# Performance work log

Hardware: AMD Instinct MI355X
Metric: run time of the kernel (lower is better)

## Reference

```python
import jax, jax.numpy as jnp
import numpy as np
import math

B, S, D, H = 2, 2048, 1024, 16
DK = D // H

def setup_inputs() -> dict:
    key = jax.random.key(0)
    ks = jax.random.split(key, 12)
    def xavier(k, shape):
        fan_in, fan_out = shape[1], shape[0]
        limit = math.sqrt(6.0 / (fan_in + fan_out))
        return jax.random.uniform(k, shape, jnp.float32, -limit, limit)
    inp = {
        'query': jax.random.normal(ks[0], (B, S, D), jnp.float32),
        'key':   jax.random.normal(ks[1], (B, S, D), jnp.float32),
        'value': jax.random.normal(ks[2], (B, S, D), jnp.float32),
        # causal mask, broadcast over heads: (B, 1, S, S), 1 = keep, 0 = mask
        'mask':  jnp.broadcast_to(jnp.tril(jnp.ones((S, S), jnp.int32)), (B, 1, S, S)),
        'Wq': xavier(ks[3], (D, D)), 'bq': jnp.zeros((D,), jnp.float32),
        'Wk': xavier(ks[4], (D, D)), 'bk': jnp.zeros((D,), jnp.float32),
        'Wv': xavier(ks[5], (D, D)), 'bv': jnp.zeros((D,), jnp.float32),
        'Wo': xavier(ks[6], (D, D)), 'bo': jnp.zeros((D,), jnp.float32),
    }
    return inp

def _split_heads(x):
    # (B, S, D) -> (B, H, S, DK)
    b, s, _ = x.shape
    return x.reshape(b, s, H, DK).transpose(0, 2, 1, 3)

def reference(query, key, value, mask, Wq, bq, Wk, bk, Wv, bv, Wo, bo):
    # torch nn.Linear: y = x @ W.T + b
    Q = _split_heads(query @ Wq.T + bq)   # (B,H,S,DK)
    K = _split_heads(key   @ Wk.T + bk)
    V = _split_heads(value @ Wv.T + bv)
    scores = jnp.einsum('bhqd,bhkd->bhqk', Q, K) / math.sqrt(DK)  # (B,H,S,S)
    scores = jnp.where(mask == 0, jnp.float32(-1e9), scores)
    attn = jax.nn.softmax(scores, axis=-1)  # dropout p=0 -> identity
    out = jnp.einsum('bhqk,bhkd->bhqd', attn, V)  # (B,H,S,DK)
    out = out.transpose(0, 2, 1, 3).reshape(query.shape[0], query.shape[1], D)
    return out @ Wo.T + bo
```

## Files before the change

kernel.cpp:

```cpp
#include <hip/hip_runtime.h>
#include <hip/hip_bf16.h>
#include <type_traits>


typedef __attribute__((ext_vector_type(8))) short short8;
typedef __attribute__((ext_vector_type(4))) short s16x4;
typedef __attribute__((ext_vector_type(4))) float floatx4;

__device__ __forceinline__ short f2bf(float x) {
    union { float f; unsigned u; } v; v.f = x;
    unsigned r = v.u + 0x7fffu + ((v.u >> 16) & 1u);
    return (short)(r >> 16);
}

__device__ __forceinline__ unsigned pk2bf(float a, float b) {
    union { __hip_bfloat162 h2; unsigned u; } cv;
    cv.h2 = __float22bfloat162_rn(make_float2(a, b));
    return cv.u;
}

__device__ __forceinline__ float fast_exp2(float x) {
#if __has_builtin(__builtin_amdgcn_exp2f)
    return __builtin_amdgcn_exp2f(x);
#else
    return __expf(x * 0.69314718056f);
#endif
}

typedef __attribute__((address_space(3))) short lds_short;
typedef __attribute__((address_space(1))) const short glb_short;
__device__ __forceinline__ void load_lds16(const void* g, void* l) {
    __builtin_amdgcn_global_load_lds((glb_short*)g, (lds_short*)l, 16, 0, 0);
}

__global__ __launch_bounds__(256) void cvt_all(
        const float* __restrict__ q, const float* __restrict__ k,
        const float* __restrict__ v,
        const float* __restrict__ wq, const float* __restrict__ wk,
        const float* __restrict__ wv, const float* __restrict__ wo,
        unsigned short* __restrict__ xq, unsigned short* __restrict__ xk,
        unsigned short* __restrict__ xv,
        unsigned short* __restrict__ wqb, unsigned short* __restrict__ wkb,
        unsigned short* __restrict__ wvb, unsigned short* __restrict__ wob) {
    const float* s; unsigned short* d;
    int bx = blockIdx.x;
    switch (blockIdx.y) {
        case 0: s = q; d = xq; break;
        case 1: s = k; d = xk; break;
        case 2: s = v; d = xv; break;
        default: {
            int wsel = bx >> 9; bx &= 511;
            s = (wsel == 0) ? wq : (wsel == 1) ? wk : (wsel == 2) ? wv : wo;
            d = (wsel == 0) ? wqb : (wsel == 1) ? wkb : (wsel == 2) ? wvb : wob;
        }
    }
    size_t i = ((size_t)bx * 256 + threadIdx.x) * 8;
    floatx4 a = *(const floatx4*)(s + i), b2 = *(const floatx4*)(s + i + 4);
    union { unsigned u[4]; short8 v8; } o;
    o.u[0] = pk2bf(a[0], a[1]);  o.u[1] = pk2bf(a[2], a[3]);
    o.u[2] = pk2bf(b2[0], b2[1]); o.u[3] = pk2bf(b2[2], b2[3]);
    *(short8*)(d + i) = o.v8;
}

__global__ __launch_bounds__(256) void gemm_qkv(
        const unsigned short* __restrict__ Xq, const unsigned short* __restrict__ Xk,
        const unsigned short* __restrict__ Xv,
        const unsigned short* __restrict__ Wq, const unsigned short* __restrict__ Wk,
        const unsigned short* __restrict__ Wv,
        const float* __restrict__ bq, const float* __restrict__ bk,
        const float* __restrict__ bv,
        unsigned short* __restrict__ Qb, unsigned short* __restrict__ Kb,
        unsigned short* __restrict__ Vb) {
    constexpr int K = 1024, N = 1024;
    __shared__ short As[128 * 64];
    __shared__ short Bs[128 * 64];
    const int t = threadIdx.x;
    const int chunk = blockIdx.y >> 5, my = blockIdx.y & 31;
    const unsigned short* A = chunk == 0 ? Xq : chunk == 1 ? Xk : Xv;
    const unsigned short* W = chunk == 0 ? Wq : chunk == 1 ? Wk : Wv;
    const float* bias        = chunk == 0 ? bq : chunk == 1 ? bk : bv;
    unsigned short* Y        = chunk == 0 ? Qb : chunk == 1 ? Kb : Vb;
    const float scale = chunk == 0 ? 0.1803368801f : 1.0f;
    const int m0 = my * 128, n0 = blockIdx.x * 128;
    const int lane = t & 63, w = t >> 6;
    const int l16 = lane & 15, quad = lane >> 4;
    const int wm = w >> 1, wn = w & 1;
    const int srow8 = t >> 3, scs8 = t & 7;
    floatx4 acc[4][4] = {};

    for (int k0 = 0; k0 < K; k0 += 64) {
        __syncthreads();
        for (int i = 0; i < 4; i++) {
            const int row = i * 32 + srow8;
            const int cg = scs8 ^ (row & 7);
            load_lds16(A + (size_t)(m0 + row) * K + k0 + cg * 8, &As[i * 2048 + t * 8]);
            load_lds16(W + (size_t)(n0 + row) * K + k0 + cg * 8, &Bs[i * 2048 + t * 8]);
        }
        __syncthreads();

        for (int kc = 0; kc < 2; kc++) {
            short8 af[4], bf[4];
            for (int ms = 0; ms < 4; ms++) {
                const int row = wm * 64 + ms * 16 + l16;
                af[ms] = *(short8*)&As[row * 64 + (((kc << 2) | quad) ^ (row & 7)) * 8];
            }
            for (int ns = 0; ns < 4; ns++) {
                const int row = wn * 64 + ns * 16 + l16;
                bf[ns] = *(short8*)&Bs[row * 64 + (((kc << 2) | quad) ^ (row & 7)) * 8];
            }
            for (int ms = 0; ms < 4; ms++)
                for (int ns = 0; ns < 4; ns++)
                    acc[ms][ns] = __builtin_amdgcn_mfma_f32_16x16x32_bf16(
                            af[ms], bf[ns], acc[ms][ns], 0, 0, 0);
        }
    }

    for (int ms = 0; ms < 4; ms++)
        for (int ns = 0; ns < 4; ns++) {
            int col = n0 + wn * 64 + ns * 16 + l16;
            float bb = bias[col];
            for (int r = 0; r < 4; r++) {
                int row = m0 + wm * 64 + ms * 16 + quad * 4 + r;
                Y[(size_t)row * N + col] =
                    (unsigned short)f2bf((acc[ms][ns][r] + bb) * scale);
            }
        }
}

__global__ __launch_bounds__(256) void gemm_o(
        const unsigned short* __restrict__ A, const unsigned short* __restrict__ W,
        float* __restrict__ P) {
    constexpr int K = 1024, N = 1024;
    __shared__ short As[128 * 64];
    __shared__ short Bs[128 * 64];
    const int t = threadIdx.x;
    const int m0 = blockIdx.y * 128, n0 = blockIdx.x * 128;
    const int kz = blockIdx.z;
    const int lane = t & 63, w = t >> 6;
    const int l16 = lane & 15, quad = lane >> 4;
    const int wm = w >> 1, wn = w & 1;
    const int srow8 = t >> 3, scs8 = t & 7;
    floatx4 acc[4][4] = {};

    for (int k0 = kz * 512; k0 < kz * 512 + 512; k0 += 64) {
        __syncthreads();
        for (int i = 0; i < 4; i++) {
            const int row = i * 32 + srow8;
            const int cg = scs8 ^ (row & 7);
            load_lds16(A + (size_t)(m0 + row) * K + k0 + cg * 8, &As[i * 2048 + t * 8]);
            load_lds16(W + (size_t)(n0 + row) * K + k0 + cg * 8, &Bs[i * 2048 + t * 8]);
        }
        __syncthreads();

        for (int kc = 0; kc < 2; kc++) {
            short8 af[4], bf[4];
            for (int ms = 0; ms < 4; ms++) {
                const int row = wm * 64 + ms * 16 + l16;
                af[ms] = *(short8*)&As[row * 64 + (((kc << 2) | quad) ^ (row & 7)) * 8];
            }
            for (int ns = 0; ns < 4; ns++) {
                const int row = wn * 64 + ns * 16 + l16;
                bf[ns] = *(short8*)&Bs[row * 64 + (((kc << 2) | quad) ^ (row & 7)) * 8];
            }
            for (int ms = 0; ms < 4; ms++)
                for (int ns = 0; ns < 4; ns++)
                    acc[ms][ns] = __builtin_amdgcn_mfma_f32_16x16x32_bf16(
                            af[ms], bf[ns], acc[ms][ns], 0, 0, 0);
        }
    }

    float* Pz = P + (size_t)kz * 4096 * N;
    for (int ms = 0; ms < 4; ms++)
        for (int ns = 0; ns < 4; ns++) {
            int col = n0 + wn * 64 + ns * 16 + l16;
            for (int r = 0; r < 4; r++) {
                int row = m0 + wm * 64 + ms * 16 + quad * 4 + r;
                Pz[(size_t)row * N + col] = acc[ms][ns][r];
            }
        }
}

__global__ __launch_bounds__(256) void reduce_o(const float* __restrict__ P,
        const float* __restrict__ bo, float* __restrict__ out) {
    size_t i = ((size_t)blockIdx.x * 256 + threadIdx.x) * 4;
    floatx4 a = *(const floatx4*)(P + i);
    floatx4 b = *(const floatx4*)(P + (size_t)4096 * 1024 + i);
    floatx4 bb = *(const floatx4*)(bo + (i & 1023));
    *(floatx4*)(out + i) = a + b + bb;
}

__global__ __launch_bounds__(256) void attn_kernel(
        const unsigned short* __restrict__ Q, const unsigned short* __restrict__ Kp,
        const unsigned short* __restrict__ Vp, unsigned short* __restrict__ O) {
    __shared__ short Ks[64 * 72];
    __shared__ short Vt[64 * 72];
    __shared__ short PsA[4][16 * 70];
    __shared__ short PsB[4][16 * 70];
    const int t = threadIdx.x;
    const int bx = blockIdx.x;
    const int unit = bx & 15, h = (bx >> 4) & 15, b = bx >> 8;
    const int q0A = unit * 64, q0B = (31 - unit) * 64;
    const int lane = t & 63, w = t >> 6, l16 = lane & 15, quad = lane >> 4;
    const int krow = t >> 2, kcg = (t & 3) * 16;
    const int vp2 = t & 31, vg = t >> 5;

    short8 qfA[2], qfB[2];
    {
        const size_t baseA = ((size_t)(b * 2048 + q0A + w * 16 + l16)) * 1024 + h * 64;
        qfA[0] = *(const short8*)(Q + baseA + quad * 8);
        qfA[1] = *(const short8*)(Q + baseA + 32 + quad * 8);
        const size_t baseB = ((size_t)(b * 2048 + q0B + w * 16 + l16)) * 1024 + h * 64;
        qfB[0] = *(const short8*)(Q + baseB + quad * 8);
        qfB[1] = *(const short8*)(Q + baseB + 32 + quad * 8);
    }
    float lA = 0.f, lB = 0.f;
    floatx4 oA[4] = {}, oB[4] = {};

    short8 ka, kb, va, vc;
    {
        const size_t kbse = ((size_t)(b * 2048 + krow)) * 1024 + h * 64 + kcg;
        ka = *(const short8*)(Kp + kbse);
        kb = *(const short8*)(Kp + kbse + 8);
        const size_t vbse = ((size_t)(b * 2048 + 2 * vp2)) * 1024 + h * 64 + vg * 8;
        va = *(const short8*)(Vp + vbse);
        vc = *(const short8*)(Vp + vbse + 1024);
    }

    for (int kv0 = 0; kv0 < q0B + 64; kv0 += 64) {
        __syncthreads();
        *(short8*)&Ks[krow * 72 + kcg] = ka;
        *(short8*)&Ks[krow * 72 + kcg + 8] = kb;
        for (int i = 0; i < 8; i++) {
            unsigned pk = (unsigned)(unsigned short)va[i] |
                          ((unsigned)(unsigned short)vc[i] << 16);
            *(unsigned*)&Vt[(vg * 8 + i) * 72 + 2 * vp2] = pk;
        }
        __syncthreads();

        if (kv0 < q0B) {
            const size_t kbse = ((size_t)(b * 2048 + kv0 + 64 + krow)) * 1024 + h * 64 + kcg;
            ka = *(const short8*)(Kp + kbse);
            kb = *(const short8*)(Kp + kbse + 8);
            const size_t vbse = ((size_t)(b * 2048 + kv0 + 64 + 2 * vp2)) * 1024 + h * 64 + vg * 8;
            va = *(const short8*)(Vp + vbse);
            vc = *(const short8*)(Vp + vbse + 1024);
        }

        auto body = [&](auto dual_c) {
            constexpr bool DUAL = decltype(dual_c)::value;
            floatx4 sB[4] = {};
            floatx4 sA[4];
            if constexpr (DUAL)
                for (int i = 0; i < 4; i++) sA[i] = (floatx4){0.f, 0.f, 0.f, 0.f};
            for (int hh = 0; hh < 4; hh++)
                for (int kc = 0; kc < 2; kc++) {
                    short8 kf = *(short8*)&Ks[(hh * 16 + l16) * 72 + kc * 32 + quad * 8];
                    sB[hh] = __builtin_amdgcn_mfma_f32_16x16x32_bf16(kf, qfB[kc], sB[hh], 0, 0, 0);
                    if constexpr (DUAL)
                        sA[hh] = __builtin_amdgcn_mfma_f32_16x16x32_bf16(kf, qfA[kc], sA[hh], 0, 0, 0);
                }

            {
                const bool needmask = (kv0 + 63 > q0B + w * 16);
                const int qg = q0B + w * 16 + l16;
                float ls = 0.f;
                for (int hh = 0; hh < 4; hh++) {
                    float p[4];
                    for (int r = 0; r < 4; r++) {
                        int kv = kv0 + hh * 16 + quad * 4 + r;
                        float e = fast_exp2(sB[hh][r]);
                        p[r] = (needmask && kv > qg) ? 0.f : e;
                        ls += p[r];
                    }
                    union { unsigned u[2]; s16x4 v4; } pw;
                    pw.u[0] = pk2bf(p[0], p[1]); pw.u[1] = pk2bf(p[2], p[3]);
                    *(s16x4*)&PsB[w][l16 * 70 + hh * 16 + quad * 4] = pw.v4;
                }
                ls += __shfl_xor(ls, 16);
                ls += __shfl_xor(ls, 32);
                lB += ls;
            }
            if constexpr (DUAL) {
                const bool needmask = (kv0 + 63 > q0A + w * 16);
                const int qg = q0A + w * 16 + l16;
                float ls = 0.f;
                for (int hh = 0; hh < 4; hh++) {
                    float p[4];
                    for (int r = 0; r < 4; r++) {
                        int kv = kv0 + hh * 16 + quad * 4 + r;
                        float e = fast_exp2(sA[hh][r]);
                        p[r] = (needmask && kv > qg) ? 0.f : e;
                        ls += p[r];
                    }
                    union { unsigned u[2]; s16x4 v4; } pw;
                    pw.u[0] = pk2bf(p[0], p[1]); pw.u[1] = pk2bf(p[2], p[3]);
                    *(s16x4*)&PsA[w][l16 * 70 + hh * 16 + quad * 4] = pw.v4;
                }
                ls += __shfl_xor(ls, 16);
                ls += __shfl_xor(ls, 32);
                lA += ls;
            }

            short8 pB0 = *(short8*)&PsB[w][l16 * 70 + quad * 8];
            short8 pB1 = *(short8*)&PsB[w][l16 * 70 + 32 + quad * 8];
            short8 pA0, pA1;
            if constexpr (DUAL) {
                pA0 = *(short8*)&PsA[w][l16 * 70 + quad * 8];
                pA1 = *(short8*)&PsA[w][l16 * 70 + 32 + quad * 8];
            }
            for (int nc = 0; nc < 4; nc++) {
                short8 vf0 = *(short8*)&Vt[(nc * 16 + l16) * 72 + quad * 8];
                short8 vf1 = *(short8*)&Vt[(nc * 16 + l16) * 72 + 32 + quad * 8];
                oB[nc] = __builtin_amdgcn_mfma_f32_16x16x32_bf16(vf0, pB0, oB[nc], 0, 0, 0);
                oB[nc] = __builtin_amdgcn_mfma_f32_16x16x32_bf16(vf1, pB1, oB[nc], 0, 0, 0);
                if constexpr (DUAL) {
                    oA[nc] = __builtin_amdgcn_mfma_f32_16x16x32_bf16(vf0, pA0, oA[nc], 0, 0, 0);
                    oA[nc] = __builtin_amdgcn_mfma_f32_16x16x32_bf16(vf1, pA1, oA[nc], 0, 0, 0);
                }
            }
        };
        if (kv0 <= q0A) body(std::integral_constant<bool, true>{});
        else            body(std::integral_constant<bool, false>{});
    }

    {
        const float rl = 1.f / lB;
        const size_t orow = ((size_t)(b * 2048 + q0B + w * 16 + l16)) * 1024 + h * 64;
        for (int nc = 0; nc < 4; nc++) {
            union { unsigned u[2]; s16x4 v4; } ow;
            ow.u[0] = pk2bf(oB[nc][0] * rl, oB[nc][1] * rl);
            ow.u[1] = pk2bf(oB[nc][2] * rl, oB[nc][3] * rl);
            *(s16x4*)(O + orow + nc * 16 + quad * 4) = ow.v4;
        }
    }
    {
        const float rl = 1.f / lA;
        const size_t orow = ((size_t)(b * 2048 + q0A + w * 16 + l16)) * 1024 + h * 64;
        for (int nc = 0; nc < 4; nc++) {
            union { unsigned u[2]; s16x4 v4; } ow;
            ow.u[0] = pk2bf(oA[nc][0] * rl, oA[nc][1] * rl);
            ow.u[1] = pk2bf(oA[nc][2] * rl, oA[nc][3] * rl);
            *(s16x4*)(O + orow + nc * 16 + quad * 4) = ow.v4;
        }
    }
}

extern "C" void kernel_launch(void* const* d_in, const int* in_sizes, int n_in,
                              void* d_out, int out_size, void* d_ws, size_t ws_size,
                              hipStream_t stream) {
    const float* query = (const float*)d_in[0];
    const float* key   = (const float*)d_in[1];
    const float* value = (const float*)d_in[2];
    const float* Wq = (const float*)d_in[4];
    const float* bq = (const float*)d_in[5];
    const float* Wk = (const float*)d_in[6];
    const float* bk = (const float*)d_in[7];
    const float* Wv = (const float*)d_in[8];
    const float* bv = (const float*)d_in[9];
    const float* Wo = (const float*)d_in[10];
    const float* bo = (const float*)d_in[11];

    const size_t NE = (size_t)4096 * 1024;
    const size_t WE = (size_t)1024 * 1024;
    unsigned short* Xq  = (unsigned short*)d_ws;
    unsigned short* Xk  = Xq + NE;
    unsigned short* Xv  = Xk + NE;
    unsigned short* Qb  = Xv + NE;
    unsigned short* Kb  = Qb + NE;
    unsigned short* Vb  = Kb + NE;
    unsigned short* Ob  = Vb + NE;
    unsigned short* Wqb = Ob + NE;
    unsigned short* Wkb = Wqb + WE;
    unsigned short* Wvb = Wkb + WE;
    unsigned short* Wob = Wvb + WE;
    float* Opart = (float*)d_ws;

    cvt_all<<<dim3(2048, 4), 256, 0, stream>>>(query, key, value, Wq, Wk, Wv, Wo,
                                               Xq, Xk, Xv, Wqb, Wkb, Wvb, Wob);
    gemm_qkv<<<dim3(8, 96), 256, 0, stream>>>(Xq, Xk, Xv, Wqb, Wkb, Wvb,
                                              bq, bk, bv, Qb, Kb, Vb);
    attn_kernel<<<dim3(512), 256, 0, stream>>>(Qb, Kb, Vb, Ob);
    gemm_o<<<dim3(8, 32, 2), 256, 0, stream>>>(Ob, Wob, Opart);
    reduce_o<<<dim3(4096), 256, 0, stream>>>(Opart, bo, (float*)d_out);
}
```

Baseline: 257.8 us.

## Split attention KV range across two blocks and drop split-K in output GEMM

The attention kernel now splits each query pair's key/value tiles between two blocks (even and odd tiles), doubling the grid to 1024 blocks. Each block writes unnormalized fp32 partial outputs and row sums, and a new combine kernel adds the halves, normalizes and converts to bf16. The output projection GEMM switches from split-K with a separate reduce kernel to 64x64 tiles over the full K, with the bias folded into its epilogue. The aim is more parallelism in attention at the cost of an extra fp32 round trip through memory. Splitting without a running max is only valid because neither half rescales against a max, so both partial sums share the same scale.

```diff
diff --git a/kernel.cpp b/kernel.cpp
--- a/kernel.cpp
+++ b/kernel.cpp
@@ -129,22 +129,21 @@
 
 __global__ __launch_bounds__(256) void gemm_o(
         const unsigned short* __restrict__ A, const unsigned short* __restrict__ W,
-        float* __restrict__ P) {
+        const float* __restrict__ bias, float* __restrict__ out) {
     constexpr int K = 1024, N = 1024;
-    __shared__ short As[128 * 64];
-    __shared__ short Bs[128 * 64];
+    __shared__ short As[64 * 64];
+    __shared__ short Bs[64 * 64];
     const int t = threadIdx.x;
-    const int m0 = blockIdx.y * 128, n0 = blockIdx.x * 128;
-    const int kz = blockIdx.z;
+    const int m0 = blockIdx.y * 64, n0 = blockIdx.x * 64;
     const int lane = t & 63, w = t >> 6;
     const int l16 = lane & 15, quad = lane >> 4;
     const int wm = w >> 1, wn = w & 1;
     const int srow8 = t >> 3, scs8 = t & 7;
-    floatx4 acc[4][4] = {};
-
-    for (int k0 = kz * 512; k0 < kz * 512 + 512; k0 += 64) {
-        __syncthreads();
-        for (int i = 0; i < 4; i++) {
+    floatx4 acc[2][2] = {};
+
+    for (int k0 = 0; k0 < K; k0 += 64) {
+        __syncthreads();
+        for (int i = 0; i < 2; i++) {
             const int row = i * 32 + srow8;
             const int cg = scs8 ^ (row & 7);
             load_lds16(A + (size_t)(m0 + row) * K + k0 + cg * 8, &As[i * 2048 + t * 8]);
@@ -153,53 +152,46 @@
         __syncthreads();
 
         for (int kc = 0; kc < 2; kc++) {
-            short8 af[4], bf[4];
-            for (int ms = 0; ms < 4; ms++) {
-                const int row = wm * 64 + ms * 16 + l16;
+            short8 af[2], bf[2];
+            for (int ms = 0; ms < 2; ms++) {
+                const int row = wm * 32 + ms * 16 + l16;
                 af[ms] = *(short8*)&As[row * 64 + (((kc << 2) | quad) ^ (row & 7)) * 8];
             }
-            for (int ns = 0; ns < 4; ns++) {
-                const int row = wn * 64 + ns * 16 + l16;
+            for (int ns = 0; ns < 2; ns++) {
+                const int row = wn * 32 + ns * 16 + l16;
                 bf[ns] = *(short8*)&Bs[row * 64 + (((kc << 2) | quad) ^ (row & 7)) * 8];
             }
-            for (int ms = 0; ms < 4; ms++)
-                for (int ns = 0; ns < 4; ns++)
+            for (int ms = 0; ms < 2; ms++)
+                for (int ns = 0; ns < 2; ns++)
                     acc[ms][ns] = __builtin_amdgcn_mfma_f32_16x16x32_bf16(
                             af[ms], bf[ns], acc[ms][ns], 0, 0, 0);
         }
     }
 
-    float* Pz = P + (size_t)kz * 4096 * N;
-    for (int ms = 0; ms < 4; ms++)
-        for (int ns = 0; ns < 4; ns++) {
-            int col = n0 + wn * 64 + ns * 16 + l16;
+    for (int ms = 0; ms < 2; ms++)
+        for (int ns = 0; ns < 2; ns++) {
+            int col = n0 + wn * 32 + ns * 16 + l16;
+            float bb = bias[col];
             for (int r = 0; r < 4; r++) {
-                int row = m0 + wm * 64 + ms * 16 + quad * 4 + r;
-                Pz[(size_t)row * N + col] = acc[ms][ns][r];
-            }
-        }
-}
-
-__global__ __launch_bounds__(256) void reduce_o(const float* __restrict__ P,
-        const float* __restrict__ bo, float* __restrict__ out) {
-    size_t i = ((size_t)blockIdx.x * 256 + threadIdx.x) * 4;
-    floatx4 a = *(const floatx4*)(P + i);
-    floatx4 b = *(const floatx4*)(P + (size_t)4096 * 1024 + i);
-    floatx4 bb = *(const floatx4*)(bo + (i & 1023));
-    *(floatx4*)(out + i) = a + b + bb;
+                int row = m0 + wm * 32 + ms * 16 + quad * 4 + r;
+                out[(size_t)row * N + col] = acc[ms][ns][r] + bb;
+            }
+        }
 }
 
 __global__ __launch_bounds__(256) void attn_kernel(
         const unsigned short* __restrict__ Q, const unsigned short* __restrict__ Kp,
-        const unsigned short* __restrict__ Vp, unsigned short* __restrict__ O) {
+        const unsigned short* __restrict__ Vp, float* __restrict__ Opart,
+        float* __restrict__ Lpart) {
     __shared__ short Ks[64 * 72];
     __shared__ short Vt[64 * 72];
     __shared__ short PsA[4][16 * 70];
     __shared__ short PsB[4][16 * 70];
     const int t = threadIdx.x;
     const int bx = blockIdx.x;
-    const int unit = bx & 15, h = (bx >> 4) & 15, b = bx >> 8;
+    const int unit = bx & 15, h = (bx >> 4) & 15, half = (bx >> 8) & 1, b = bx >> 9;
     const int q0A = unit * 64, q0B = (31 - unit) * 64;
+    const int nB = 32 - unit;
     const int lane = t & 63, w = t >> 6, l16 = lane & 15, quad = lane >> 4;
     const int krow = t >> 2, kcg = (t & 3) * 16;
     const int vp2 = t & 31, vg = t >> 5;
@@ -218,15 +210,16 @@
 
     short8 ka, kb, va, vc;
     {
-        const size_t kbse = ((size_t)(b * 2048 + krow)) * 1024 + h * 64 + kcg;
+        const size_t kbse = ((size_t)(b * 2048 + half * 64 + krow)) * 1024 + h * 64 + kcg;
         ka = *(const short8*)(Kp + kbse);
         kb = *(const short8*)(Kp + kbse + 8);
-        const size_t vbse = ((size_t)(b * 2048 + 2 * vp2)) * 1024 + h * 64 + vg * 8;
+        const size_t vbse = ((size_t)(b * 2048 + half * 64 + 2 * vp2)) * 1024 + h * 64 + vg * 8;
         va = *(const short8*)(Vp + vbse);
         vc = *(const short8*)(Vp + vbse + 1024);
     }
 
-    for (int kv0 = 0; kv0 < q0B + 64; kv0 += 64) {
+    for (int kvt = half; kvt < nB; kvt += 2) {
+        const int kv0 = kvt * 64;
         __syncthreads();
         *(short8*)&Ks[krow * 72 + kcg] = ka;
         *(short8*)&Ks[krow * 72 + kcg + 8] = kb;
@@ -237,11 +230,12 @@
         }
         __syncthreads();
 
-        if (kv0 < q0B) {
-            const size_t kbse = ((size_t)(b * 2048 + kv0 + 64 + krow)) * 1024 + h * 64 + kcg;
+        if (kvt + 2 < nB) {
+            const int nx = (kvt + 2) * 64;
+            const size_t kbse = ((size_t)(b * 2048 + nx + krow)) * 1024 + h * 64 + kcg;
             ka = *(const short8*)(Kp + kbse);
             kb = *(const short8*)(Kp + kbse + 8);
-            const size_t vbse = ((size_t)(b * 2048 + kv0 + 64 + 2 * vp2)) * 1024 + h * 64 + vg * 8;
+            const size_t vbse = ((size_t)(b * 2048 + nx + 2 * vp2)) * 1024 + h * 64 + vg * 8;
             va = *(const short8*)(Vp + vbse);
             vc = *(const short8*)(Vp + vbse + 1024);
         }
@@ -323,26 +317,34 @@
         else            body(std::integral_constant<bool, false>{});
     }
 
+    float* Oh = Opart + (size_t)half * 4194304;
     {
-        const float rl = 1.f / lB;
-        const size_t orow = ((size_t)(b * 2048 + q0B + w * 16 + l16)) * 1024 + h * 64;
-        for (int nc = 0; nc < 4; nc++) {
-            union { unsigned u[2]; s16x4 v4; } ow;
-            ow.u[0] = pk2bf(oB[nc][0] * rl, oB[nc][1] * rl);
-            ow.u[1] = pk2bf(oB[nc][2] * rl, oB[nc][3] * rl);
-            *(s16x4*)(O + orow + nc * 16 + quad * 4) = ow.v4;
-        }
+        const int rowg = b * 2048 + q0B + w * 16 + l16;
+        float* Op = Oh + (size_t)rowg * 1024 + h * 64;
+        for (int nc = 0; nc < 4; nc++)
+            *(floatx4*)(Op + nc * 16 + quad * 4) = oB[nc];
+        if (quad == 0) Lpart[half * 65536 + rowg * 16 + h] = lB;
     }
     {
-        const float rl = 1.f / lA;
-        const size_t orow = ((size_t)(b * 2048 + q0A + w * 16 + l16)) * 1024 + h * 64;
-        for (int nc = 0; nc < 4; nc++) {
-            union { unsigned u[2]; s16x4 v4; } ow;
-            ow.u[0] = pk2bf(oA[nc][0] * rl, oA[nc][1] * rl);
-            ow.u[1] = pk2bf(oA[nc][2] * rl, oA[nc][3] * rl);
-            *(s16x4*)(O + orow + nc * 16 + quad * 4) = ow.v4;
-        }
-    }
+        const int rowg = b * 2048 + q0A + w * 16 + l16;
+        float* Op = Oh + (size_t)rowg * 1024 + h * 64;
+        for (int nc = 0; nc < 4; nc++)
+            *(floatx4*)(Op + nc * 16 + quad * 4) = oA[nc];
+        if (quad == 0) Lpart[half * 65536 + rowg * 16 + h] = lA;
+    }
+}
+
+__global__ __launch_bounds__(256) void combine_o(const float* __restrict__ Op,
+        const float* __restrict__ Lp, unsigned short* __restrict__ Ob) {
+    size_t i = ((size_t)blockIdx.x * 256 + threadIdx.x) * 4;
+    int row = (int)(i >> 10), h = ((int)i >> 6) & 15;
+    floatx4 a = *(const floatx4*)(Op + i);
+    floatx4 b = *(const floatx4*)(Op + 4194304 + i);
+    float rl = 1.f / (Lp[row * 16 + h] + Lp[65536 + row * 16 + h]);
+    union { unsigned u[2]; s16x4 v4; } ow;
+    ow.u[0] = pk2bf((a[0] + b[0]) * rl, (a[1] + b[1]) * rl);
+    ow.u[1] = pk2bf((a[2] + b[2]) * rl, (a[3] + b[3]) * rl);
+    *(s16x4*)(Ob + i) = ow.v4;
 }
 
 extern "C" void kernel_launch(void* const* d_in, const int* in_sizes, int n_in,
@@ -360,26 +362,26 @@
     const float* Wo = (const float*)d_in[10];
     const float* bo = (const float*)d_in[11];
 
-    const size_t NE = (size_t)4096 * 1024;
-    const size_t WE = (size_t)1024 * 1024;
-    unsigned short* Xq  = (unsigned short*)d_ws;
-    unsigned short* Xk  = Xq + NE;
-    unsigned short* Xv  = Xk + NE;
-    unsigned short* Qb  = Xv + NE;
-    unsigned short* Kb  = Qb + NE;
-    unsigned short* Vb  = Kb + NE;
-    unsigned short* Ob  = Vb + NE;
-    unsigned short* Wqb = Ob + NE;
-    unsigned short* Wkb = Wqb + WE;
-    unsigned short* Wvb = Wkb + WE;
-    unsigned short* Wob = Wvb + WE;
-    float* Opart = (float*)d_ws;
+    unsigned short* base = (unsigned short*)d_ws;
+    unsigned short* Qb  = base;
+    unsigned short* Kb  = base + 4194304;
+    unsigned short* Vb  = base + 8388608;
+    unsigned short* Ob  = Kb;
+    unsigned short* Wob = base + 12582912;
+    float* Lpart = (float*)(base + 13631488);
+    float* Opart = (float*)((char*)d_ws + (size_t)28 * 1024 * 1024);
+    unsigned short* Xq  = base + 14680064;
+    unsigned short* Xk  = base + 18874368;
+    unsigned short* Xv  = base + 23068672;
+    unsigned short* Wqb = base + 27262976;
+    unsigned short* Wkb = base + 28311552;
+    unsigned short* Wvb = base + 29360128;
 
     cvt_all<<<dim3(2048, 4), 256, 0, stream>>>(query, key, value, Wq, Wk, Wv, Wo,
                                                Xq, Xk, Xv, Wqb, Wkb, Wvb, Wob);
     gemm_qkv<<<dim3(8, 96), 256, 0, stream>>>(Xq, Xk, Xv, Wqb, Wkb, Wvb,
                                               bq, bk, bv, Qb, Kb, Vb);
-    attn_kernel<<<dim3(512), 256, 0, stream>>>(Qb, Kb, Vb, Ob);
-    gemm_o<<<dim3(8, 32, 2), 256, 0, stream>>>(Ob, Wob, Opart);
-    reduce_o<<<dim3(4096), 256, 0, stream>>>(Opart, bo, (float*)d_out);
-}
+    attn_kernel<<<dim3(1024), 256, 0, stream>>>(Qb, Kb, Vb, Opart, Lpart);
+    combine_o<<<dim3(4096), 256, 0, stream>>>(Opart, Lpart, Ob);
+    gemm_o<<<dim3(16, 64), 256, 0, stream>>>(Ob, Wob, bo, (float*)d_out);
+}
```

After: 259.7 us. No clear change (+0.8%).

## Fuse activation bf16 conversion into QKV GEMM and drop split-K output reduction

Applied to the files above, without the earlier changes.

The QKV projection GEMM now reads fp32 activations directly, converting them to bf16 in registers with a one-tile register prefetch before storing to LDS. This removes the separate conversion pass over the three activation tensors. The output projection switches from a 128x128 split-K GEMM plus a reduce kernel to 64x64 tiles over the full K, with the bias added in the epilogue. That removes the fp32 partial-sum round trip and one launch, at the cost of synchronous global loads in the QKV loop and smaller, less reuse-efficient tiles in the output GEMM.

```diff
diff --git a/kernel.cpp b/kernel.cpp
--- a/kernel.cpp
+++ b/kernel.cpp
@@ -33,38 +33,29 @@
     __builtin_amdgcn_global_load_lds((glb_short*)g, (lds_short*)l, 16, 0, 0);
 }
 
-__global__ __launch_bounds__(256) void cvt_all(
-        const float* __restrict__ q, const float* __restrict__ k,
-        const float* __restrict__ v,
-        const float* __restrict__ wq, const float* __restrict__ wk,
-        const float* __restrict__ wv, const float* __restrict__ wo,
-        unsigned short* __restrict__ xq, unsigned short* __restrict__ xk,
-        unsigned short* __restrict__ xv,
-        unsigned short* __restrict__ wqb, unsigned short* __restrict__ wkb,
-        unsigned short* __restrict__ wvb, unsigned short* __restrict__ wob) {
+__global__ __launch_bounds__(256) void cvt_w(
+        const float* __restrict__ s0, const float* __restrict__ s1,
+        const float* __restrict__ s2, const float* __restrict__ s3,
+        unsigned short* __restrict__ d0, unsigned short* __restrict__ d1,
+        unsigned short* __restrict__ d2, unsigned short* __restrict__ d3) {
     const float* s; unsigned short* d;
-    int bx = blockIdx.x;
     switch (blockIdx.y) {
-        case 0: s = q; d = xq; break;
-        case 1: s = k; d = xk; break;
-        case 2: s = v; d = xv; break;
-        default: {
-            int wsel = bx >> 9; bx &= 511;
-            s = (wsel == 0) ? wq : (wsel == 1) ? wk : (wsel == 2) ? wv : wo;
-            d = (wsel == 0) ? wqb : (wsel == 1) ? wkb : (wsel == 2) ? wvb : wob;
-        }
-    }
-    size_t i = ((size_t)bx * 256 + threadIdx.x) * 8;
+        case 0: s = s0; d = d0; break;
+        case 1: s = s1; d = d1; break;
+        case 2: s = s2; d = d2; break;
+        default: s = s3; d = d3; break;
+    }
+    size_t i = ((size_t)blockIdx.x * 256 + threadIdx.x) * 8;
     floatx4 a = *(const floatx4*)(s + i), b2 = *(const floatx4*)(s + i + 4);
     union { unsigned u[4]; short8 v8; } o;
-    o.u[0] = pk2bf(a[0], a[1]);  o.u[1] = pk2bf(a[2], a[3]);
+    o.u[0] = pk2bf(a[0], a[1]);   o.u[1] = pk2bf(a[2], a[3]);
     o.u[2] = pk2bf(b2[0], b2[1]); o.u[3] = pk2bf(b2[2], b2[3]);
     *(short8*)(d + i) = o.v8;
 }
 
 __global__ __launch_bounds__(256) void gemm_qkv(
-        const unsigned short* __restrict__ Xq, const unsigned short* __restrict__ Xk,
-        const unsigned short* __restrict__ Xv,
+        const float* __restrict__ Xq, const float* __restrict__ Xk,
+        const float* __restrict__ Xv,
         const unsigned short* __restrict__ Wq, const unsigned short* __restrict__ Wk,
         const unsigned short* __restrict__ Wv,
         const float* __restrict__ bq, const float* __restrict__ bk,
@@ -76,10 +67,10 @@
     __shared__ short Bs[128 * 64];
     const int t = threadIdx.x;
     const int chunk = blockIdx.y >> 5, my = blockIdx.y & 31;
-    const unsigned short* A = chunk == 0 ? Xq : chunk == 1 ? Xk : Xv;
+    const float* A    = chunk == 0 ? Xq : chunk == 1 ? Xk : Xv;
     const unsigned short* W = chunk == 0 ? Wq : chunk == 1 ? Wk : Wv;
-    const float* bias        = chunk == 0 ? bq : chunk == 1 ? bk : bv;
-    unsigned short* Y        = chunk == 0 ? Qb : chunk == 1 ? Kb : Vb;
+    const float* bias = chunk == 0 ? bq : chunk == 1 ? bk : bv;
+    unsigned short* Y = chunk == 0 ? Qb : chunk == 1 ? Kb : Vb;
     const float scale = chunk == 0 ? 0.1803368801f : 1.0f;
     const int m0 = my * 128, n0 = blockIdx.x * 128;
     const int lane = t & 63, w = t >> 6;
@@ -88,13 +79,37 @@
     const int srow8 = t >> 3, scs8 = t & 7;
     floatx4 acc[4][4] = {};
 
+    floatx4 pa[4][2];
+    for (int i = 0; i < 4; i++) {
+        const int row = i * 32 + srow8;
+        const float* ap = A + (size_t)(m0 + row) * K + (scs8 ^ (row & 7)) * 8;
+        pa[i][0] = *(const floatx4*)ap;
+        pa[i][1] = *(const floatx4*)(ap + 4);
+    }
+
     for (int k0 = 0; k0 < K; k0 += 64) {
         __syncthreads();
         for (int i = 0; i < 4; i++) {
             const int row = i * 32 + srow8;
-            const int cg = scs8 ^ (row & 7);
-            load_lds16(A + (size_t)(m0 + row) * K + k0 + cg * 8, &As[i * 2048 + t * 8]);
-            load_lds16(W + (size_t)(n0 + row) * K + k0 + cg * 8, &Bs[i * 2048 + t * 8]);
+            load_lds16(W + (size_t)(n0 + row) * K + k0 + ((scs8 ^ (row & 7))) * 8,
+                       &Bs[i * 2048 + t * 8]);
+        }
+        for (int i = 0; i < 4; i++) {
+            union { unsigned u[4]; short8 v8; } o;
+            o.u[0] = pk2bf(pa[i][0][0], pa[i][0][1]);
+            o.u[1] = pk2bf(pa[i][0][2], pa[i][0][3]);
+            o.u[2] = pk2bf(pa[i][1][0], pa[i][1][1]);
+            o.u[3] = pk2bf(pa[i][1][2], pa[i][1][3]);
+            *(short8*)&As[i * 2048 + t * 8] = o.v8;
+        }
+        if (k0 + 64 < K) {
+            for (int i = 0; i < 4; i++) {
+                const int row = i * 32 + srow8;
+                const float* ap = A + (size_t)(m0 + row) * K + (k0 + 64) +
+                                  (scs8 ^ (row & 7)) * 8;
+                pa[i][0] = *(const floatx4*)ap;
+                pa[i][1] = *(const floatx4*)(ap + 4);
+            }
         }
         __syncthreads();
 
@@ -129,22 +144,21 @@
 
 __global__ __launch_bounds__(256) void gemm_o(
         const unsigned short* __restrict__ A, const unsigned short* __restrict__ W,
-        float* __restrict__ P) {
+        const float* __restrict__ bias, float* __restrict__ out) {
     constexpr int K = 1024, N = 1024;
-    __shared__ short As[128 * 64];
-    __shared__ short Bs[128 * 64];
+    __shared__ short As[64 * 64];
+    __shared__ short Bs[64 * 64];
     const int t = threadIdx.x;
-    const int m0 = blockIdx.y * 128, n0 = blockIdx.x * 128;
-    const int kz = blockIdx.z;
+    const int m0 = blockIdx.y * 64, n0 = blockIdx.x * 64;
     const int lane = t & 63, w = t >> 6;
     const int l16 = lane & 15, quad = lane >> 4;
     const int wm = w >> 1, wn = w & 1;
     const int srow8 = t >> 3, scs8 = t & 7;
-    floatx4 acc[4][4] = {};
-
-    for (int k0 = kz * 512; k0 < kz * 512 + 512; k0 += 64) {
-        __syncthreads();
-        for (int i = 0; i < 4; i++) {
+    floatx4 acc[2][2] = {};
+
+    for (int k0 = 0; k0 < K; k0 += 64) {
+        __syncthreads();
+        for (int i = 0; i < 2; i++) {
             const int row = i * 32 + srow8;
             const int cg = scs8 ^ (row & 7);
             load_lds16(A + (size_t)(m0 + row) * K + k0 + cg * 8, &As[i * 2048 + t * 8]);
@@ -153,40 +167,31 @@
         __syncthreads();
 
         for (int kc = 0; kc < 2; kc++) {
-            short8 af[4], bf[4];
-            for (int ms = 0; ms < 4; ms++) {
-                const int row = wm * 64 + ms * 16 + l16;
+            short8 af[2], bf[2];
+            for (int ms = 0; ms < 2; ms++) {
+                const int row = wm * 32 + ms * 16 + l16;
                 af[ms] = *(short8*)&As[row * 64 + (((kc << 2) | quad) ^ (row & 7)) * 8];
             }
-            for (int ns = 0; ns < 4; ns++) {
-                const int row = wn * 64 + ns * 16 + l16;
+            for (int ns = 0; ns < 2; ns++) {
+                const int row = wn * 32 + ns * 16 + l16;
                 bf[ns] = *(short8*)&Bs[row * 64 + (((kc << 2) | quad) ^ (row & 7)) * 8];
             }
-            for (int ms = 0; ms < 4; ms++)
-                for (int ns = 0; ns < 4; ns++)
+            for (int ms = 0; ms < 2; ms++)
+                for (int ns = 0; ns < 2; ns++)
                     acc[ms][ns] = __builtin_amdgcn_mfma_f32_16x16x32_bf16(
                             af[ms], bf[ns], acc[ms][ns], 0, 0, 0);
         }
     }
 
-    float* Pz = P + (size_t)kz * 4096 * N;
-    for (int ms = 0; ms < 4; ms++)
-        for (int ns = 0; ns < 4; ns++) {
-            int col = n0 + wn * 64 + ns * 16 + l16;
+    for (int ms = 0; ms < 2; ms++)
+        for (int ns = 0; ns < 2; ns++) {
+            int col = n0 + wn * 32 + ns * 16 + l16;
+            float bb = bias[col];
             for (int r = 0; r < 4; r++) {
-                int row = m0 + wm * 64 + ms * 16 + quad * 4 + r;
-                Pz[(size_t)row * N + col] = acc[ms][ns][r];
-            }
-        }
-}
-
-__global__ __launch_bounds__(256) void reduce_o(const float* __restrict__ P,
-        const float* __restrict__ bo, float* __restrict__ out) {
-    size_t i = ((size_t)blockIdx.x * 256 + threadIdx.x) * 4;
-    floatx4 a = *(const floatx4*)(P + i);
-    floatx4 b = *(const floatx4*)(P + (size_t)4096 * 1024 + i);
-    floatx4 bb = *(const floatx4*)(bo + (i & 1023));
-    *(floatx4*)(out + i) = a + b + bb;
+                int row = m0 + wm * 32 + ms * 16 + quad * 4 + r;
+                out[(size_t)row * N + col] = acc[ms][ns][r] + bb;
+            }
+        }
 }
 
 __global__ __launch_bounds__(256) void attn_kernel(
@@ -362,10 +367,7 @@
 
     const size_t NE = (size_t)4096 * 1024;
     const size_t WE = (size_t)1024 * 1024;
-    unsigned short* Xq  = (unsigned short*)d_ws;
-    unsigned short* Xk  = Xq + NE;
-    unsigned short* Xv  = Xk + NE;
-    unsigned short* Qb  = Xv + NE;
+    unsigned short* Qb  = (unsigned short*)d_ws;
     unsigned short* Kb  = Qb + NE;
     unsigned short* Vb  = Kb + NE;
     unsigned short* Ob  = Vb + NE;
@@ -373,13 +375,10 @@
     unsigned short* Wkb = Wqb + WE;
     unsigned short* Wvb = Wkb + WE;
     unsigned short* Wob = Wvb + WE;
-    float* Opart = (float*)d_ws;
-
-    cvt_all<<<dim3(2048, 4), 256, 0, stream>>>(query, key, value, Wq, Wk, Wv, Wo,
-                                               Xq, Xk, Xv, Wqb, Wkb, Wvb, Wob);
-    gemm_qkv<<<dim3(8, 96), 256, 0, stream>>>(Xq, Xk, Xv, Wqb, Wkb, Wvb,
+
+    cvt_w<<<dim3(512, 4), 256, 0, stream>>>(Wq, Wk, Wv, Wo, Wqb, Wkb, Wvb, Wob);
+    gemm_qkv<<<dim3(8, 96), 256, 0, stream>>>(query, key, value, Wqb, Wkb, Wvb,
                                               bq, bk, bv, Qb, Kb, Vb);
     attn_kernel<<<dim3(512), 256, 0, stream>>>(Qb, Kb, Vb, Ob);
-    gemm_o<<<dim3(8, 32, 2), 256, 0, stream>>>(Ob, Wob, Opart);
-    reduce_o<<<dim3(4096), 256, 0, stream>>>(Opart, bo, (float*)d_out);
-}
+    gemm_o<<<dim3(16, 64), 256, 0, stream>>>(Ob, Wob, bo, (float*)d_out);
+}
```

After: 269.4 us. +4.5%, slower.
